# Kernel optimization log

Hardware: AMD Instinct MI355X
Metric: run time of the kernel (lower is better)

## Reference

```python
import jax, jax.numpy as jnp
import numpy as np

N_USER, N_MOVIE = 100000, 20000
D_USER, D_MOVIE = 32, 64
H = 64
E = 2000000
B = 200000


def _sage(x_src, x_dst, src, dst, W_l, b_l, W_r, n_dst):
    # PyG SAGEConv: out = lin_l(mean_{j in N(i)} x_j) + lin_r(x_i)
    msg = x_src[src]                                   # [E, d_src] gather
    agg = jax.ops.segment_sum(msg, dst, num_segments=n_dst)
    cnt = jax.ops.segment_sum(jnp.ones((src.shape[0],), x_src.dtype), dst,
                              num_segments=n_dst)
    mean = agg / jnp.maximum(cnt, 1.0)[:, None]        # [n_dst, d_src]
    return mean @ W_l + b_l + x_dst @ W_r


def setup_inputs() -> dict:
    key = jax.random.key(0)
    ks = jax.random.split(key, 24)
    f = jnp.float32

    def lin(k, din, dout):
        s = 1.0 / np.sqrt(din)
        return jax.random.uniform(k, (din, dout), f, -s, s)

    inp = {
        'x_user': jax.random.normal(ks[0], (N_USER, D_USER), f),
        'x_movie': jax.random.normal(ks[1], (N_MOVIE, D_MOVIE), f),
        'src_um': jax.random.randint(ks[2], (E,), 0, N_USER),
        'dst_um': jax.random.randint(ks[3], (E,), 0, N_MOVIE),
        'src_mu': jax.random.randint(ks[4], (E,), 0, N_MOVIE),
        'dst_mu': jax.random.randint(ks[5], (E,), 0, N_USER),
        'label_row': jax.random.randint(ks[6], (B,), 0, N_USER),
        'label_col': jax.random.randint(ks[7], (B,), 0, N_MOVIE),
        # layer 1, edge type user->movie (dst=movie): lin_l on aggregated src (user feats)
        'W1_um_l': lin(ks[8], D_USER, H), 'b1_um': jnp.zeros((H,), f),
        'W1_um_r': lin(ks[9], D_MOVIE, H),
        # layer 1, edge type movie->user (dst=user)
        'W1_mu_l': lin(ks[10], D_MOVIE, H), 'b1_mu': jnp.zeros((H,), f),
        'W1_mu_r': lin(ks[11], D_USER, H),
        # layer 2 (inputs are hidden H for both types)
        'W2_um_l': lin(ks[12], H, H), 'b2_um': jnp.zeros((H,), f),
        'W2_um_r': lin(ks[13], H, H),
        'W2_mu_l': lin(ks[14], H, H), 'b2_mu': jnp.zeros((H,), f),
        'W2_mu_r': lin(ks[15], H, H),
        # head: Linear(2H, 2)
        'W_lin': lin(ks[16], 2 * H, 2), 'b_lin': jnp.zeros((2,), f),
    }
    return inp


def reference(x_user, x_movie, src_um, dst_um, src_mu, dst_mu,
              label_row, label_col,
              W1_um_l, b1_um, W1_um_r, W1_mu_l, b1_mu, W1_mu_r,
              W2_um_l, b2_um, W2_um_r, W2_mu_l, b2_mu, W2_mu_r,
              W_lin, b_lin):
    # layer 1 (to_hetero aggr='sum': each node type has one incoming edge type)
    h_movie = _sage(x_user, x_movie, src_um, dst_um, W1_um_l, b1_um, W1_um_r, N_MOVIE)
    h_user = _sage(x_movie, x_user, src_mu, dst_mu, W1_mu_l, b1_mu, W1_mu_r, N_USER)
    h_movie = jax.nn.relu(h_movie)
    h_user = jax.nn.relu(h_user)
    # layer 2
    z_movie = _sage(h_user, h_movie, src_um, dst_um, W2_um_l, b2_um, W2_um_r, N_MOVIE)
    z_user = _sage(h_movie, h_user, src_mu, dst_mu, W2_mu_l, b2_mu, W2_mu_r, N_USER)
    # head
    concat = jnp.concatenate([z_user[label_row], z_movie[label_col]], axis=-1)
    out = concat @ W_lin + b_lin                       # [B, 2]
    mu = out[:, 0]
    sigma = jax.nn.softplus(out[:, 1]) + 1e-6
    return mu, sigma
```

## Files before the change

kernel.cpp:

```cpp
#include <hip/hip_runtime.h>
#include <hip/hip_bf16.h>
#include <hip/hip_fp16.h>
#include <type_traits>

#define NB_UM 157
#define NB_MU 196
#define NBALL 353
#define NBLK 256

using f16x8 = __attribute__((ext_vector_type(8))) _Float16;
using f32x4 = __attribute__((ext_vector_type(4))) float;


__global__ __launch_bounds__(256) void cast_half2(const float* __restrict__ a,
                                                  __half* __restrict__ ah, int na,
                                                  const float* __restrict__ b,
                                                  __half* __restrict__ bh, int nb) {
    int i = blockIdx.x * blockDim.x + threadIdx.x;
    int st = gridDim.x * blockDim.x;
    for (int k = i; k < na / 2; k += st) {
        float2 v = ((const float2*)a)[k];
        ((__half2*)ah)[k] = __floats2half2_rn(v.x, v.y);
    }
    for (int k = i; k < nb / 2; k += st) {
        float2 v = ((const float2*)b)[k];
        ((__half2*)bh)[k] = __floats2half2_rn(v.x, v.y);
    }
}


__global__ __launch_bounds__(1024) void hist_part(const int* __restrict__ dst_um,
                                                  const int* __restrict__ dst_mu,
                                                  int* __restrict__ histM, int E) {
    __shared__ int h[NBALL];
    for (int i = threadIdx.x; i < NBALL; i += 1024) h[i] = 0;
    __syncthreads();
    int blk = blockIdx.x;
    int chunk = (E + NBLK - 1) / NBLK;
    int s = blk * chunk, e = min(E, s + chunk);
    for (int i = s + threadIdx.x; i < e; i += 1024) {
        atomicAdd(&h[dst_um[i] >> 7], 1);
        atomicAdd(&h[NB_UM + (dst_mu[i] >> 9)], 1);
    }
    __syncthreads();
    for (int i = threadIdx.x; i < NBALL; i += 1024) histM[i * NBLK + blk] = h[i];
}


__global__ __launch_bounds__(256) void bucket_totals(int* __restrict__ histM,
                                                     int* __restrict__ btot, int nball) {
    int w = (blockIdx.x * blockDim.x + threadIdx.x) >> 6;
    int lane = threadIdx.x & 63;
    if (w >= nball) return;
    int* row = histM + w * NBLK;
    int v[4];
    int s = 0;
#pragma unroll
    for (int i = 0; i < 4; i++) {
        int c = row[lane * 4 + i];
        v[i] = s;
        s += c;
    }
    int incl = s;
    for (int d = 1; d < 64; d <<= 1) {
        int y = __shfl_up(incl, d, 64);
        if (lane >= d) incl += y;
    }
    int excl = incl - s;
#pragma unroll
    for (int i = 0; i < 4; i++) row[lane * 4 + i] = excl + v[i];
    if (lane == 63) btot[w] = incl;
}


__global__ __launch_bounds__(256) void boff_scan(const int* __restrict__ btot,
                                                 int* __restrict__ boff, int nball,
                                                 int* __restrict__ off_um, int NM,
                                                 int* __restrict__ off_mu, int NU, int E) {
    __shared__ int sdata[256];
    int t = threadIdx.x;
    int v[8];
    int sum = 0;
#pragma unroll
    for (int i = 0; i < 8; i++) {
        int idx = t * 8 + i;
        int c = (idx < nball) ? btot[idx] : 0;
        v[i] = sum;
        sum += c;
    }
    sdata[t] = sum;
    __syncthreads();
    for (int s = 1; s < 256; s <<= 1) {
        int y = (t >= s) ? sdata[t - s] : 0;
        __syncthreads();
        sdata[t] += y;
        __syncthreads();
    }
    int base = (t == 0) ? 0 : sdata[t - 1];
#pragma unroll
    for (int i = 0; i < 8; i++) {
        int idx = t * 8 + i;
        if (idx < nball) boff[idx] = base + v[i];
    }
    if (t == 0) {
        boff[nball] = 2 * E;
        off_um[NM] = E;
        off_mu[NU] = E;
    }
}


__global__ __launch_bounds__(256) void add_boff(int* __restrict__ histM,
                                                const int* __restrict__ boff, int n) {
    int st = gridDim.x * blockDim.x;
    for (int i = blockIdx.x * blockDim.x + threadIdx.x; i < n; i += st)
        histM[i] += boff[i >> 8];
}


__global__ __launch_bounds__(1024) void partition2(const int* __restrict__ src_um,
                                                   const int* __restrict__ dst_um,
                                                   const int* __restrict__ src_mu,
                                                   const int* __restrict__ dst_mu,
                                                   const int* __restrict__ histM,
                                                   int* __restrict__ tmp, int E) {
    __shared__ int cur[NBALL];
    int blk = blockIdx.x;
    for (int i = threadIdx.x; i < NBALL; i += 1024) cur[i] = histM[i * NBLK + blk];
    __syncthreads();
    int chunk = (E + NBLK - 1) / NBLK;
    int s = blk * chunk, e = min(E, s + chunk);
    for (int i = s + threadIdx.x; i < e; i += 1024) {
        int d = dst_um[i];
        int p = atomicAdd(&cur[d >> 7], 1);
        tmp[p] = src_um[i] | ((d & 127) << 20);
        int d2 = dst_mu[i];
        int q = atomicAdd(&cur[NB_MU ? (NB_UM + (d2 >> 9)) : 0], 1);
        tmp[q] = src_mu[i] | ((d2 & 511) << 20);
    }
}


template <int W>
__global__ __launch_bounds__(1024) void scatter_csr(const int* __restrict__ tmp,
                                                    const int* __restrict__ boff,
                                                    int* __restrict__ off,
                                                    int* __restrict__ csr, int n, int sub) {
    __shared__ int lcnt[W];
    __shared__ int lcur[W];
    __shared__ int sdata[1024];
    int b = blockIdx.x;
    int t = threadIdx.x;
    int s = boff[b], e = boff[b + 1];
    for (int j = t; j < W; j += 1024) lcnt[j] = 0;
    __syncthreads();
    for (int i = s + t; i < e; i += 1024) atomicAdd(&lcnt[tmp[i] >> 20], 1);
    __syncthreads();
    int myc = (t < W) ? lcnt[t] : 0;
    sdata[t] = myc;
    __syncthreads();
    for (int d = 1; d < 1024; d <<= 1) {
        int y = (t >= d) ? sdata[t - d] : 0;
        __syncthreads();
        sdata[t] += y;
        __syncthreads();
    }
    if (t < W) lcur[t] = s + sdata[t] - myc;
    __syncthreads();
    int rowbase = b * W;
    for (int j = t; j < W; j += 1024)
        if (rowbase + j < n) off[rowbase + j] = lcur[j] - sub;
    __syncthreads();
    for (int i = s + t; i < e; i += 1024) {
        int vv = tmp[i];
        int p = atomicAdd(&lcur[vv >> 20], 1);
        csr[p - sub] = vv & 0xFFFFF;
    }
}


__device__ __forceinline__ void acc8(float* a, uint4 r) {
    const __half2* h = reinterpret_cast<const __half2*>(&r);
#pragma unroll
    for (int j = 0; j < 4; j++) {
        float2 f = __half22float2(h[j]);
        a[2 * j] += f.x;
        a[2 * j + 1] += f.y;
    }
}

template <int D>
__global__ __launch_bounds__(256) void agg_mean_g(const int* __restrict__ csr,
                                                  const int* __restrict__ off,
                                                  const __half* __restrict__ xh,
                                                  float* __restrict__ out, int nrows) {
    constexpr int L = D / 8;
    int gid = (blockIdx.x * blockDim.x + threadIdx.x) / L;
    int lg = threadIdx.x & (L - 1);
    int ngroups = (gridDim.x * blockDim.x) / L;
    int c8 = lg * 8;
    for (int row = gid; row < nrows; row += ngroups) {
        int s = off[row], e = off[row + 1];
        float a[8] = {0.f, 0.f, 0.f, 0.f, 0.f, 0.f, 0.f, 0.f};
        int k = s;
        for (; k + 4 <= e; k += 4) {
            int i0 = csr[k], i1 = csr[k + 1], i2 = csr[k + 2], i3 = csr[k + 3];
            uint4 r0 = *(const uint4*)&xh[(long)i0 * D + c8];
            uint4 r1 = *(const uint4*)&xh[(long)i1 * D + c8];
            uint4 r2 = *(const uint4*)&xh[(long)i2 * D + c8];
            uint4 r3 = *(const uint4*)&xh[(long)i3 * D + c8];
            acc8(a, r0); acc8(a, r1); acc8(a, r2); acc8(a, r3);
        }
        for (; k < e; ++k) {
            uint4 r0 = *(const uint4*)&xh[(long)csr[k] * D + c8];
            acc8(a, r0);
        }
        float inv = 1.0f / fmaxf((float)(e - s), 1.0f);
        float4 q0 = make_float4(a[0] * inv, a[1] * inv, a[2] * inv, a[3] * inv);
        float4 q1 = make_float4(a[4] * inv, a[5] * inv, a[6] * inv, a[7] * inv);
        *(float4*)&out[(long)row * D + c8] = q0;
        *(float4*)&out[(long)row * D + c8 + 4] = q1;
    }
}


template <int Dm, int Dd, bool RELU, typename TX, typename TO>
__global__ __launch_bounds__(256) void dense_mfma(const float* __restrict__ mean,
                                                  const TX* __restrict__ xd,
                                                  const float* __restrict__ Wl,
                                                  const float* __restrict__ Wr,
                                                  const float* __restrict__ bias,
                                                  TO* __restrict__ out, int n) {
    constexpr int K = Dm + Dd;
    constexpr int SAP = K + 8;
    __shared__ __align__(16) _Float16 sA[64 * SAP];
    __shared__ __align__(16) _Float16 sWt[64 * SAP];
    __shared__ float sb[64];
    int t = threadIdx.x;
    int R0 = blockIdx.x * 64;

    for (int i = t; i < K * 16; i += 256) {
        int k = i >> 4, c = (i & 15) * 4;
        float4 v = (k < Dm) ? *(const float4*)&Wl[k * 64 + c]
                            : *(const float4*)&Wr[(k - Dm) * 64 + c];
        sWt[(c + 0) * SAP + k] = (_Float16)v.x;
        sWt[(c + 1) * SAP + k] = (_Float16)v.y;
        sWt[(c + 2) * SAP + k] = (_Float16)v.z;
        sWt[(c + 3) * SAP + k] = (_Float16)v.w;
    }
    if (t < 64) sb[t] = bias[t];
    constexpr int QR = K / 4;
    for (int i = t; i < 64 * QR; i += 256) {
        int r = i / QR, c = (i % QR) * 4;
        int gr = R0 + r;
        float4 v = make_float4(0.f, 0.f, 0.f, 0.f);
        if (gr < n) {
            if (c < Dm) {
                v = *(const float4*)&mean[(long)gr * Dm + c];
            } else {
                if constexpr (std::is_same<TX, __half>::value) {
                    const __half* p = &xd[(long)gr * Dd + (c - Dm)];
                    v = make_float4(__half2float(p[0]), __half2float(p[1]),
                                    __half2float(p[2]), __half2float(p[3]));
                } else {
                    v = *(const float4*)&xd[(long)gr * Dd + (c - Dm)];
                }
            }
        }
        _Float16* p = &sA[r * SAP + c];
        p[0] = (_Float16)v.x; p[1] = (_Float16)v.y;
        p[2] = (_Float16)v.z; p[3] = (_Float16)v.w;
    }
    __syncthreads();

    int w = t >> 6, lane = t & 63;
    int lr = lane & 15, lg = lane >> 4;
    f32x4 acc[4];
#pragma unroll
    for (int nt = 0; nt < 4; nt++) {
        float bb = sb[16 * nt + lr];
        acc[nt][0] = bb; acc[nt][1] = bb; acc[nt][2] = bb; acc[nt][3] = bb;
    }
    int arow = 16 * w + lr;
#pragma unroll
    for (int kk = 0; kk < K / 32; kk++) {
        int k0 = kk * 32 + 8 * lg;
        f16x8 a = *(const f16x8*)&sA[arow * SAP + k0];
#pragma unroll
        for (int nt = 0; nt < 4; nt++) {
            f16x8 b = *(const f16x8*)&sWt[(16 * nt + lr) * SAP + k0];
            acc[nt] = __builtin_amdgcn_mfma_f32_16x16x32_f16(a, b, acc[nt], 0, 0, 0);
        }
    }
#pragma unroll
    for (int nt = 0; nt < 4; nt++) {
#pragma unroll
        for (int r = 0; r < 4; r++) {
            int gr = R0 + 16 * w + lg * 4 + r;
            if (gr >= n) continue;
            float vv = acc[nt][r];
            if (RELU) vv = fmaxf(vv, 0.f);
            int gc = 16 * nt + lr;
            if constexpr (std::is_same<TO, __half>::value) {
                out[(long)gr * 64 + gc] = __float2half(vv);
            } else {
                out[(long)gr * 64 + gc] = vv;
            }
        }
    }
}


__global__ __launch_bounds__(256) void proj_kernel(const float* __restrict__ z,
                                                   const float* __restrict__ Wlin,
                                                   int woff, const float* __restrict__ blin,
                                                   int addb, float2* __restrict__ p, int n) {
    __shared__ float sW0[64], sW1[64];
    int t = threadIdx.x;
    if (t < 64) {
        sW0[t] = Wlin[(woff + t) * 2 + 0];
        sW1[t] = Wlin[(woff + t) * 2 + 1];
    }
    __syncthreads();
    float b0 = addb ? blin[0] : 0.f;
    float b1 = addb ? blin[1] : 0.f;
    int lane = t & 63;
    int w = t >> 6;
    int lr = lane & 15, q = lane >> 4;
    int row = blockIdx.x * 16 + w * 4 + q;
    if (row >= n) return;
    float4 zv = *(const float4*)&z[(long)row * 64 + lr * 4];
    float p0 = zv.x * sW0[lr * 4] + zv.y * sW0[lr * 4 + 1] + zv.z * sW0[lr * 4 + 2] + zv.w * sW0[lr * 4 + 3];
    float p1 = zv.x * sW1[lr * 4] + zv.y * sW1[lr * 4 + 1] + zv.z * sW1[lr * 4 + 2] + zv.w * sW1[lr * 4 + 3];
#pragma unroll
    for (int m = 1; m < 16; m <<= 1) {
        p0 += __shfl_xor(p0, m, 64);
        p1 += __shfl_xor(p1, m, 64);
    }
    if (lr == 0) p[row] = make_float2(p0 + b0, p1 + b1);
}


__global__ __launch_bounds__(256) void head_gather(const float2* __restrict__ pu,
                                                   const float2* __restrict__ pm,
                                                   const int* __restrict__ lrow,
                                                   const int* __restrict__ lcol,
                                                   float* __restrict__ out, int B) {
    int i = blockIdx.x * blockDim.x + threadIdx.x;
    int st = gridDim.x * blockDim.x;
    for (int b = i; b < B; b += st) {
        float2 a = pu[lrow[b]];
        float2 d = pm[lcol[b]];
        float m = a.x + d.x;
        float x = a.y + d.y;
        float sp = fmaxf(x, 0.f) + log1pf(expf(-fabsf(x)));
        out[b] = m;
        out[B + b] = sp + 1e-6f;
    }
}


extern "C" void kernel_launch(void* const* d_in, const int* in_sizes, int n_in,
                              void* d_out, int out_size, void* d_ws, size_t ws_size,
                              hipStream_t stream) {
    const float* x_user  = (const float*)d_in[0];
    const float* x_movie = (const float*)d_in[1];
    const int* src_um = (const int*)d_in[2];
    const int* dst_um = (const int*)d_in[3];
    const int* src_mu = (const int*)d_in[4];
    const int* dst_mu = (const int*)d_in[5];
    const int* lrow = (const int*)d_in[6];
    const int* lcol = (const int*)d_in[7];
    const float* W1_um_l = (const float*)d_in[8];
    const float* b1_um   = (const float*)d_in[9];
    const float* W1_um_r = (const float*)d_in[10];
    const float* W1_mu_l = (const float*)d_in[11];
    const float* b1_mu   = (const float*)d_in[12];
    const float* W1_mu_r = (const float*)d_in[13];
    const float* W2_um_l = (const float*)d_in[14];
    const float* b2_um   = (const float*)d_in[15];
    const float* W2_um_r = (const float*)d_in[16];
    const float* W2_mu_l = (const float*)d_in[17];
    const float* b2_mu   = (const float*)d_in[18];
    const float* W2_mu_r = (const float*)d_in[19];
    const float* W_lin   = (const float*)d_in[20];
    const float* b_lin   = (const float*)d_in[21];
    float* out = (float*)d_out;

    const int E  = in_sizes[2];
    const int B  = in_sizes[6];
    const int NU = in_sizes[0] / 32;
    const int NM = in_sizes[1] / 64;

    char* wsp = (char*)d_ws;
    size_t o = 0;
    auto alloc = [&](size_t bytes) {
        size_t p = o;
        o += (bytes + 255) & ~(size_t)255;
        return (void*)(wsp + p);
    };
    int* off_um = (int*)alloc((size_t)(NM + 1) * 4);
    int* off_mu = (int*)alloc((size_t)(NU + 1) * 4);
    int* btot   = (int*)alloc((NBALL) * 4);
    int* boff   = (int*)alloc((NBALL + 1) * 4);
    int* csr_um = (int*)alloc((size_t)E * 4);
    int* csr_mu = (int*)alloc((size_t)E * 4);
    float* A_m  = (float*)alloc((size_t)NM * 64 * 4);
    float* A_u  = (float*)alloc((size_t)NU * 64 * 4);
    __half* Hh_m = (__half*)alloc((size_t)NM * 64 * 2);
    __half* Hh_u = (__half*)alloc((size_t)NU * 64 * 2);
    __half* xh_u = (__half*)alloc((size_t)NU * 32 * 2);
    __half* xh_m = (__half*)alloc((size_t)NM * 64 * 2);
    float2* pu  = (float2*)alloc((size_t)NU * 8);
    float2* pm  = (float2*)alloc((size_t)NM * 8);
    (void)ws_size;

    int* tmp   = (int*)A_u;
    int* histM = (int*)A_m;

    cast_half2<<<512, 256, 0, stream>>>(x_user, xh_u, NU * 32, x_movie, xh_m, NM * 64);

    hist_part<<<NBLK, 1024, 0, stream>>>(dst_um, dst_mu, histM, E);
    bucket_totals<<<(NBALL + 3) / 4, 256, 0, stream>>>(histM, btot, NBALL);
    boff_scan<<<1, 256, 0, stream>>>(btot, boff, NBALL, off_um, NM, off_mu, NU, E);
    add_boff<<<352, 256, 0, stream>>>(histM, boff, NBALL * NBLK);
    partition2<<<NBLK, 1024, 0, stream>>>(src_um, dst_um, src_mu, dst_mu, histM, tmp, E);
    scatter_csr<128><<<NB_UM, 1024, 0, stream>>>(tmp, boff, off_um, csr_um, NM, 0);
    scatter_csr<512><<<NB_MU, 1024, 0, stream>>>(tmp, boff + NB_UM, off_mu, csr_mu, NU, E);

    agg_mean_g<32><<<(NM * 4 + 255) / 256, 256, 0, stream>>>(csr_um, off_um, xh_u, A_m, NM);
    dense_mfma<32, 64, true, float, __half><<<(NM + 63) / 64, 256, 0, stream>>>(
        A_m, x_movie, W1_um_l, W1_um_r, b1_um, Hh_m, NM);
    agg_mean_g<64><<<(NU * 8 + 255) / 256, 256, 0, stream>>>(csr_mu, off_mu, xh_m, A_u, NU);
    dense_mfma<64, 32, true, float, __half><<<(NU + 63) / 64, 256, 0, stream>>>(
        A_u, x_user, W1_mu_l, W1_mu_r, b1_mu, Hh_u, NU);

    agg_mean_g<64><<<(NM * 8 + 255) / 256, 256, 0, stream>>>(csr_um, off_um, Hh_u, A_m, NM);
    dense_mfma<64, 64, false, __half, float><<<(NM + 63) / 64, 256, 0, stream>>>(
        A_m, Hh_m, W2_um_l, W2_um_r, b2_um, A_m, NM);
    agg_mean_g<64><<<(NU * 8 + 255) / 256, 256, 0, stream>>>(csr_mu, off_mu, Hh_m, A_u, NU);
    dense_mfma<64, 64, false, __half, float><<<(NU + 63) / 64, 256, 0, stream>>>(
        A_u, Hh_u, W2_mu_l, W2_mu_r, b2_mu, A_u, NU);

    proj_kernel<<<(NU + 15) / 16, 256, 0, stream>>>(A_u, W_lin, 0, b_lin, 1, pu, NU);
    proj_kernel<<<(NM + 15) / 16, 256, 0, stream>>>(A_m, W_lin, 64, b_lin, 0, pm, NM);
    head_gather<<<1024, 256, 0, stream>>>(pu, pm, lrow, lcol, out, B);
}
```

Measured before the change: 270.2 us.

## Fuse CSR build kernels, vectorize edge loads, fold bucket offsets into partition

```diff
diff --git a/kernel.cpp b/kernel.cpp
--- a/kernel.cpp
+++ b/kernel.cpp
@@ -31,16 +31,32 @@
 
 __global__ __launch_bounds__(1024) void hist_part(const int* __restrict__ dst_um,
                                                   const int* __restrict__ dst_mu,
-                                                  int* __restrict__ histM, int E) {
+                                                  int* __restrict__ histM, int E, int chunk) {
     __shared__ int h[NBALL];
     for (int i = threadIdx.x; i < NBALL; i += 1024) h[i] = 0;
     __syncthreads();
     int blk = blockIdx.x;
-    int chunk = (E + NBLK - 1) / NBLK;
     int s = blk * chunk, e = min(E, s + chunk);
-    for (int i = s + threadIdx.x; i < e; i += 1024) {
-        atomicAdd(&h[dst_um[i] >> 7], 1);
-        atomicAdd(&h[NB_UM + (dst_mu[i] >> 9)], 1);
+    if (s < e) {
+        int n4 = (e - s) >> 2;
+        const int4* du4 = (const int4*)(dst_um + s);
+        const int4* dm4 = (const int4*)(dst_mu + s);
+        for (int i = threadIdx.x; i < n4; i += 1024) {
+            int4 d = du4[i];
+            atomicAdd(&h[d.x >> 7], 1);
+            atomicAdd(&h[d.y >> 7], 1);
+            atomicAdd(&h[d.z >> 7], 1);
+            atomicAdd(&h[d.w >> 7], 1);
+            int4 m = dm4[i];
+            atomicAdd(&h[NB_UM + (m.x >> 9)], 1);
+            atomicAdd(&h[NB_UM + (m.y >> 9)], 1);
+            atomicAdd(&h[NB_UM + (m.z >> 9)], 1);
+            atomicAdd(&h[NB_UM + (m.w >> 9)], 1);
+        }
+        for (int i = s + (n4 << 2) + threadIdx.x; i < e; i += 1024) {
+            atomicAdd(&h[dst_um[i] >> 7], 1);
+            atomicAdd(&h[NB_UM + (dst_mu[i] >> 9)], 1);
+        }
     }
     __syncthreads();
     for (int i = threadIdx.x; i < NBALL; i += 1024) histM[i * NBLK + blk] = h[i];
@@ -110,46 +126,68 @@
 }
 
 
-__global__ __launch_bounds__(256) void add_boff(int* __restrict__ histM,
-                                                const int* __restrict__ boff, int n) {
-    int st = gridDim.x * blockDim.x;
-    for (int i = blockIdx.x * blockDim.x + threadIdx.x; i < n; i += st)
-        histM[i] += boff[i >> 8];
-}
-
-
 __global__ __launch_bounds__(1024) void partition2(const int* __restrict__ src_um,
                                                    const int* __restrict__ dst_um,
                                                    const int* __restrict__ src_mu,
                                                    const int* __restrict__ dst_mu,
                                                    const int* __restrict__ histM,
-                                                   int* __restrict__ tmp, int E) {
+                                                   const int* __restrict__ boff,
+                                                   int* __restrict__ tmp, int E, int chunk) {
     __shared__ int cur[NBALL];
     int blk = blockIdx.x;
-    for (int i = threadIdx.x; i < NBALL; i += 1024) cur[i] = histM[i * NBLK + blk];
-    __syncthreads();
-    int chunk = (E + NBLK - 1) / NBLK;
+    for (int i = threadIdx.x; i < NBALL; i += 1024)
+        cur[i] = histM[i * NBLK + blk] + boff[i];
+    __syncthreads();
     int s = blk * chunk, e = min(E, s + chunk);
-    for (int i = s + threadIdx.x; i < e; i += 1024) {
+    if (s >= e) return;
+    int n4 = (e - s) >> 2;
+    const int4* su4 = (const int4*)(src_um + s);
+    const int4* du4 = (const int4*)(dst_um + s);
+    const int4* sm4 = (const int4*)(src_mu + s);
+    const int4* dm4 = (const int4*)(dst_mu + s);
+    for (int i = threadIdx.x; i < n4; i += 1024) {
+        int4 sv = su4[i];
+        int4 dv = du4[i];
+        int p;
+        p = atomicAdd(&cur[dv.x >> 7], 1); tmp[p] = sv.x | ((dv.x & 127) << 20);
+        p = atomicAdd(&cur[dv.y >> 7], 1); tmp[p] = sv.y | ((dv.y & 127) << 20);
+        p = atomicAdd(&cur[dv.z >> 7], 1); tmp[p] = sv.z | ((dv.z & 127) << 20);
+        p = atomicAdd(&cur[dv.w >> 7], 1); tmp[p] = sv.w | ((dv.w & 127) << 20);
+        int4 sv2 = sm4[i];
+        int4 dv2 = dm4[i];
+        p = atomicAdd(&cur[NB_UM + (dv2.x >> 9)], 1); tmp[p] = sv2.x | ((dv2.x & 511) << 20);
+        p = atomicAdd(&cur[NB_UM + (dv2.y >> 9)], 1); tmp[p] = sv2.y | ((dv2.y & 511) << 20);
+        p = atomicAdd(&cur[NB_UM + (dv2.z >> 9)], 1); tmp[p] = sv2.z | ((dv2.z & 511) << 20);
+        p = atomicAdd(&cur[NB_UM + (dv2.w >> 9)], 1); tmp[p] = sv2.w | ((dv2.w & 511) << 20);
+    }
+    for (int i = s + (n4 << 2) + threadIdx.x; i < e; i += 1024) {
         int d = dst_um[i];
         int p = atomicAdd(&cur[d >> 7], 1);
         tmp[p] = src_um[i] | ((d & 127) << 20);
         int d2 = dst_mu[i];
-        int q = atomicAdd(&cur[NB_MU ? (NB_UM + (d2 >> 9)) : 0], 1);
+        int q = atomicAdd(&cur[NB_UM + (d2 >> 9)], 1);
         tmp[q] = src_mu[i] | ((d2 & 511) << 20);
     }
 }
 
 
-template <int W>
-__global__ __launch_bounds__(1024) void scatter_csr(const int* __restrict__ tmp,
-                                                    const int* __restrict__ boff,
-                                                    int* __restrict__ off,
-                                                    int* __restrict__ csr, int n, int sub) {
-    __shared__ int lcnt[W];
-    __shared__ int lcur[W];
+__global__ __launch_bounds__(1024) void scatter_both(const int* __restrict__ tmp,
+                                                     const int* __restrict__ boff,
+                                                     int* __restrict__ off_um,
+                                                     int* __restrict__ csr_um, int NM,
+                                                     int* __restrict__ off_mu,
+                                                     int* __restrict__ csr_mu, int NU, int E) {
+    __shared__ int lcnt[512];
+    __shared__ int lcur[512];
     __shared__ int sdata[1024];
     int b = blockIdx.x;
+    int um = (b < NB_UM);
+    int W = um ? 128 : 512;
+    int n = um ? NM : NU;
+    int sub = um ? 0 : E;
+    int* off = um ? off_um : off_mu;
+    int* csr = um ? csr_um : csr_mu;
+    int rowbase = (um ? b : (b - NB_UM)) * W;
     int t = threadIdx.x;
     int s = boff[b], e = boff[b + 1];
     for (int j = t; j < W; j += 1024) lcnt[j] = 0;
@@ -167,7 +205,6 @@
     }
     if (t < W) lcur[t] = s + sdata[t] - myc;
     __syncthreads();
-    int rowbase = b * W;
     for (int j = t; j < W; j += 1024)
         if (rowbase + j < n) off[rowbase + j] = lcur[j] - sub;
     __syncthreads();
@@ -418,15 +455,17 @@
     int* tmp   = (int*)A_u;
     int* histM = (int*)A_m;
 
+    const int chunk = (((E + NBLK - 1) / NBLK) + 3) & ~3;
+
     cast_half2<<<512, 256, 0, stream>>>(x_user, xh_u, NU * 32, x_movie, xh_m, NM * 64);
 
-    hist_part<<<NBLK, 1024, 0, stream>>>(dst_um, dst_mu, histM, E);
+    hist_part<<<NBLK, 1024, 0, stream>>>(dst_um, dst_mu, histM, E, chunk);
     bucket_totals<<<(NBALL + 3) / 4, 256, 0, stream>>>(histM, btot, NBALL);
     boff_scan<<<1, 256, 0, stream>>>(btot, boff, NBALL, off_um, NM, off_mu, NU, E);
-    add_boff<<<352, 256, 0, stream>>>(histM, boff, NBALL * NBLK);
-    partition2<<<NBLK, 1024, 0, stream>>>(src_um, dst_um, src_mu, dst_mu, histM, tmp, E);
-    scatter_csr<128><<<NB_UM, 1024, 0, stream>>>(tmp, boff, off_um, csr_um, NM, 0);
-    scatter_csr<512><<<NB_MU, 1024, 0, stream>>>(tmp, boff + NB_UM, off_mu, csr_mu, NU, E);
+    partition2<<<NBLK, 1024, 0, stream>>>(src_um, dst_um, src_mu, dst_mu, histM, boff,
+                                          tmp, E, chunk);
+    scatter_both<<<NBALL, 1024, 0, stream>>>(tmp, boff, off_um, csr_um, NM,
+                                             off_mu, csr_mu, NU, E);
 
     agg_mean_g<32><<<(NM * 4 + 255) / 256, 256, 0, stream>>>(csr_um, off_um, xh_u, A_m, NM);
     dense_mfma<32, 64, true, float, __half><<<(NM + 63) / 64, 256, 0, stream>>>(
```

New measurement: 262.2 us. -2.9%, faster.
